# Performance work log

Hardware: AMD Instinct MI355X
Metric: run time of the kernel (lower is better)

The kernel has to match this reference:

```python
import jax, jax.numpy as jnp
import numpy as np


def setup_inputs() -> dict:
    key = jax.random.key(0)
    k1, k2 = jax.random.split(key)
    visual_features = jax.random.normal(k1, (16, 1024, 768), dtype=jnp.float32)
    text_tokens = jax.random.normal(k2, (16, 256, 768), dtype=jnp.float32)
    return {"visual_features": visual_features, "text_tokens": text_tokens, "k": 16}


def reference(visual_features, text_tokens, k):
    B, N, D = visual_features.shape
    T = min(k, N)

    # normalize (note: norm + 1e-6 in denominator, matching torch code)
    vis_norm = visual_features / (jnp.linalg.norm(visual_features, axis=-1, keepdims=True) + 1e-6)
    vis_norm = vis_norm.astype(jnp.float32)
    txt_norm = text_tokens / (jnp.linalg.norm(text_tokens, axis=-1, keepdims=True) + 1e-6)
    txt_norm = txt_norm.astype(jnp.float32)

    similarity = jnp.einsum('bnd,bmd->bnm', vis_norm, vis_norm)          # (B,N,N)
    relevance = jnp.einsum('bnd,btd->bnt', vis_norm, txt_norm).max(-1)    # (B,N)
    r_min = relevance.min(axis=1, keepdims=True)
    r_max = relevance.max(axis=1, keepdims=True)
    relevance = (relevance - r_min + 1e-6) / (r_max - r_min + 1e-6)

    kernel = relevance[:, :, None] * similarity * relevance[:, None, :]   # (B,N,N)

    di2s0 = jnp.diagonal(kernel, axis1=1, axis2=2)                        # (B,N)
    cis0 = jnp.zeros((T, B, N), dtype=kernel.dtype)
    barange = jnp.arange(B)

    def step(carry, i):
        di2s, cis = carry
        safe = jnp.maximum(di2s, 1e-12)
        j = jnp.argmax(safe, axis=-1)                                     # (B,)
        k_j = jnp.take_along_axis(kernel, j[:, None, None], axis=1)[:, 0, :]  # (B,N)
        dj = jnp.take_along_axis(di2s, j[:, None], axis=1)[:, 0]          # (B,)
        denom = jnp.sqrt(jnp.maximum(dj, 1e-12))[:, None] + 1e-8          # (B,1)
        # cis rows >= i are zero, so full-T contraction equals contraction over :i
        c_tb = jnp.take_along_axis(cis, j[None, :, None], axis=2)[:, :, 0]  # (T,B)
        cov = jnp.einsum('tb,tbn->bn', c_tb, cis)                         # (B,N)
        eis = (k_j - cov) / denom                                         # (B,N)
        cis = jax.lax.dynamic_update_index_in_dim(cis, eis, i, axis=0)
        di2s = di2s - eis ** 2
        di2s = di2s.at[barange, j].set(-jnp.inf)
        return (di2s, cis), j

    (_, _), sel = jax.lax.scan(step, (di2s0, cis0), jnp.arange(T))        # sel: (T,B)
    select_idx = jnp.sort(sel.T, axis=1)                                  # (B,T)
    selected = jnp.take_along_axis(visual_features, select_idx[:, :, None], axis=1)  # (B,T,D)
    if T < k:
        pad = jnp.zeros((B, k - T, D), dtype=selected.dtype)
        selected = jnp.concatenate([selected, pad], axis=1)
    return selected
```

## Files before the change

### kernel.cpp

```cpp
#include <hip/hip_runtime.h>
#include <math.h>

#define NB 16
#define NN 1024
#define ND 768
#define NT 256
#define NSEL 16
#define NC 64

typedef __attribute__((ext_vector_type(8))) short short8;
typedef __attribute__((ext_vector_type(4))) float f32x4;
typedef __attribute__((ext_vector_type(8))) unsigned short ushort8v;
typedef unsigned long long u64;

__device__ __align__(16) float g_invv[NB*NN];
__device__ __align__(16) float g_diagv[NB*NN];
__device__ __align__(16) float g_mrawp[NB*NN*2];
__device__ __align__(16) ushort8v g_tf[NB*2*24*2*8*64];

__device__ __forceinline__ unsigned short f2bf(float x) {
    unsigned u = __float_as_uint(x);
    return (unsigned short)((u + 0x7FFFu + ((u >> 16) & 1u)) >> 16);
}
__device__ __forceinline__ float bf2f(unsigned short h) {
    return __uint_as_float(((unsigned)h) << 16);
}
__device__ __forceinline__ size_t tfidx(int b, int th, int s, int h, int ct, int lane) {
    return ((((size_t)(b*2 + th)*24 + s)*2 + h)*8 + ct)*64 + lane;
}

__global__ __launch_bounds__(256) void ktxt(const float* __restrict__ txt) {
    int gw = (blockIdx.x * 256 + threadIdx.x) >> 6;
    int l  = threadIdx.x & 63;
    int b  = gw >> 8, r = gw & 255;
    int th = r >> 7, ct = (r >> 4) & 7, rlo = r & 15;
    const float* row = txt + (size_t)gw * ND;

    float4 x0 = *(const float4*)(row + 8*l);
    float4 y0 = *(const float4*)(row + 8*l + 4);
    float4 x1 = {0,0,0,0}, y1 = {0,0,0,0};
    bool two = (l < 32);
    if (two) {
        x1 = *(const float4*)(row + 512 + 8*l);
        y1 = *(const float4*)(row + 512 + 8*l + 4);
    }
    float s = x0.x*x0.x + x0.y*x0.y + x0.z*x0.z + x0.w*x0.w
            + y0.x*y0.x + y0.y*y0.y + y0.z*y0.z + y0.w*y0.w;
    if (two) s += x1.x*x1.x + x1.y*x1.y + x1.z*x1.z + x1.w*x1.w
                + y1.x*y1.x + y1.y*y1.y + y1.z*y1.z + y1.w*y1.w;
    #pragma unroll
    for (int off = 32; off; off >>= 1) s += __shfl_xor(s, off);
    float inv = 1.0f / (sqrtf(s) + 1e-6f);

    int kslot = l & 3;
    int lane  = kslot*16 + rlo;
    {
        int st = l >> 2;
        float a[8] = {x0.x, x0.y, x0.z, x0.w, y0.x, y0.y, y0.z, y0.w};
        ushort8v hh, ll;
        #pragma unroll
        for (int j = 0; j < 8; j++) {
            float v = a[j] * inv;
            hh[j] = f2bf(v);
            ll[j] = f2bf(v - bf2f(hh[j]));
        }
        g_tf[tfidx(b, th, st, 0, ct, lane)] = hh;
        g_tf[tfidx(b, th, st, 1, ct, lane)] = ll;
    }
    if (two) {
        int st = 16 + (l >> 2);
        float a[8] = {x1.x, x1.y, x1.z, x1.w, y1.x, y1.y, y1.z, y1.w};
        ushort8v hh, ll;
        #pragma unroll
        for (int j = 0; j < 8; j++) {
            float v = a[j] * inv;
            hh[j] = f2bf(v);
            ll[j] = f2bf(v - bf2f(hh[j]));
        }
        g_tf[tfidx(b, th, st, 0, ct, lane)] = hh;
        g_tf[tfidx(b, th, st, 1, ct, lane)] = ll;
    }
}

__global__ __launch_bounds__(256) void krel(const float* __restrict__ vis) {
    int bid = blockIdx.x;
    int lid = (bid & 7) * 64 + (bid >> 3);
    int b   = lid >> 5;
    int mt  = (lid >> 1) & 15;
    int th  = lid & 1;
    int t   = threadIdx.x;
    int w   = t >> 6, l = t & 63;

    __shared__ __align__(16) ushort8v Bfrag[3][2][8][64];

    f32x4 acc[8];
    #pragma unroll
    for (int ct = 0; ct < 8; ct++) acc[ct] = (f32x4){0.f, 0.f, 0.f, 0.f};

    int arow = mt*64 + w*16 + (l & 15);
    int akq  = (l >> 4) * 8;
    const float* Ap = vis + ((size_t)(b*NN + arow))*ND + akq;

    const ushort8v* Bbase = g_tf + tfidx(b, th, 0, 0, 0, 0);

    #define STAGE(S, P)                                                          \
        {                                                                        \
            _Pragma("unroll")                                                    \
            for (int q = 0; q < 4; q++) {                                        \
                int c  = w*4 + q;                                                \
                int h  = c >> 3, ct = c & 7;                                     \
                const ushort8v* gsrc = Bbase + (((size_t)(S)*2 + h)*8 + ct)*64 + l; \
                __builtin_amdgcn_global_load_lds(                                \
                    (const __attribute__((address_space(1))) void*)gsrc,         \
                    (__attribute__((address_space(3))) void*)&Bfrag[P][h][ct][0],\
                    16, 0, 0);                                                   \
            }                                                                    \
        }

    float4 rax = *(const float4*)(Ap);
    float4 ray = *(const float4*)(Ap + 4);
    STAGE(0, 0);
    STAGE(1, 1);
    __syncthreads();
    float ss = 0.f;

    for (int s = 0; s < 24; s++) {
        int p = s % 3;
        int k0 = s * 32;
        if (s < 22) STAGE(s + 2, (s + 2) % 3);
        asm volatile("" ::: "memory");
        float av[8] = {rax.x, rax.y, rax.z, rax.w, ray.x, ray.y, ray.z, ray.w};
        ushort8v hh, ll;
        #pragma unroll
        for (int j = 0; j < 8; j++) {
            hh[j] = f2bf(av[j]);
            ll[j] = f2bf(av[j] - bf2f(hh[j]));
            ss = fmaf(av[j], av[j], ss);
        }
        short8 ah = *(short8*)&hh;
        short8 al = *(short8*)&ll;
        if (s < 23) {
            rax = *(const float4*)(Ap + k0 + 32);
            ray = *(const float4*)(Ap + k0 + 36);
        }
        #pragma unroll
        for (int ct = 0; ct < 8; ct++) {
            short8 bh = *(const short8*)&Bfrag[p][0][ct][l];
            short8 bl = *(const short8*)&Bfrag[p][1][ct][l];
            acc[ct] = __builtin_amdgcn_mfma_f32_16x16x32_bf16(ah, bh, acc[ct], 0, 0, 0);
            acc[ct] = __builtin_amdgcn_mfma_f32_16x16x32_bf16(al, bh, acc[ct], 0, 0, 0);
            acc[ct] = __builtin_amdgcn_mfma_f32_16x16x32_bf16(ah, bl, acc[ct], 0, 0, 0);
            acc[ct] = __builtin_amdgcn_mfma_f32_16x16x32_bf16(al, bl, acc[ct], 0, 0, 0);
        }
        if (s < 23) {
            asm volatile("s_waitcnt lgkmcnt(0)" ::: "memory");
            __builtin_amdgcn_s_barrier();
            __builtin_amdgcn_sched_barrier(0);
        }
    }
    #undef STAGE

    #pragma unroll
    for (int r = 0; r < 4; r++) {
        float m = acc[0][r];
        #pragma unroll
        for (int ct = 1; ct < 8; ct++) m = fmaxf(m, acc[ct][r]);
        #pragma unroll
        for (int off = 1; off <= 8; off <<= 1) m = fmaxf(m, __shfl_xor(m, off));
        if ((l & 15) == 0)
            g_mrawp[(size_t)(b*NN + mt*64 + w*16 + (l >> 4)*4 + r)*2 + th] = m;
    }

    ss += __shfl_xor(ss, 16);
    ss += __shfl_xor(ss, 32);
    if (th == 0 && l < 16) {
        int row = mt*64 + w*16 + l;
        float nrm = sqrtf(ss);
        float inv = 1.0f / (nrm + 1e-6f);
        g_invv[b*NN + row] = inv;
        float dd = nrm * inv;
        g_diagv[b*NN + row] = dd * dd;
    }
}

__global__ __launch_bounds__(1024) void kfinal(const float* __restrict__ vis,
                                               float* __restrict__ out) {
    int b = blockIdx.x;
    int t = threadIdx.x;
    int w = t >> 6, l = t & 63;

    __shared__ u64   s_key[NN];
    __shared__ float s_reln[NN];
    __shared__ __align__(16) unsigned short Chi[NC][392], Clo[NC][392];
    __shared__ float s_S[NC*65];
    __shared__ int   s_sel[NSEL], s_srt[NSEL];
    __shared__ float s_mn[16], s_mx[16], s_b2[2];

    float m0 = g_mrawp[(size_t)(b*NN + t)*2 + 0];
    float m1 = g_mrawp[(size_t)(b*NN + t)*2 + 1];
    float iv = g_invv[b*NN + t], dd = g_diagv[b*NN + t];
    float rr = fmaxf(m0, m1) * iv;
    float lmin = rr, lmax = rr;
    #pragma unroll
    for (int off = 32; off; off >>= 1) {
        lmin = fminf(lmin, __shfl_xor(lmin, off));
        lmax = fmaxf(lmax, __shfl_xor(lmax, off));
    }
    if (l == 0) { s_mn[w] = lmin; s_mx[w] = lmax; }
    __syncthreads();
    if (t == 0) {
        float mn = s_mn[0], mx = s_mx[0];
        #pragma unroll
        for (int q = 1; q < 16; q++) { mn = fminf(mn, s_mn[q]); mx = fmaxf(mx, s_mx[q]); }
        s_b2[0] = mn; s_b2[1] = mx;
    }
    __syncthreads();
    float mn = s_b2[0], mx = s_b2[1];
    float den = mx - mn + 1e-6f;
    float rn = (rr - mn + 1e-6f) / den;
    float d0 = rn * rn * dd;
    s_reln[t] = rn;
    u64 kreg = ((u64)(~__float_as_uint(d0)) << 10) | (unsigned)t;

    #pragma unroll
    for (int k = 2; k <= 64; k <<= 1) {
        #pragma unroll
        for (int j = k >> 1; j > 0; j >>= 1) {
            u64 part = __shfl_xor(kreg, j);
            bool takeMin = ((l & k) == 0) == ((l & j) == 0);
            kreg = takeMin ? (kreg < part ? kreg : part) : (kreg < part ? part : kreg);
        }
    }
    #pragma unroll
    for (int rnd = 0; rnd < 4; rnd++) {
        int dstp = 8 >> rnd;
        s_key[w*64 + l] = kreg;
        __syncthreads();
        u64 other = s_key[(w ^ dstp)*64 + (63 - l)];
        u64 m = (kreg < other) ? kreg : other;
        #pragma unroll
        for (int j = 32; j > 0; j >>= 1) {
            u64 part = __shfl_xor(m, j);
            bool takeMin = ((l & j) == 0);
            m = takeMin ? (m < part ? m : part) : (m < part ? part : m);
        }
        kreg = m;
        __syncthreads();
    }

    int   gid = (int)(kreg & 1023u);
    float d0v = __uint_as_float(~(unsigned)(kreg >> 10));

    f32x4 acc = (f32x4){0.f, 0.f, 0.f, 0.f};
    int ar0 = (w >> 2) * 16, bc0 = (w & 3) * 16;
    int cr  = (w << 2) + (l >> 4);
    int sgid = __shfl(gid, cr);
    float sc = g_invv[b*NN + sgid];
    const float* srcrow = vis + (size_t)(b*NN + sgid)*ND + (l & 15)*24;

    for (int c = 0; c < 2; c++) {
        __syncthreads();
        int kb = (l & 15) * 24;
        #pragma unroll
        for (int q = 0; q < 3; q++) {
            float4 x = *(const float4*)(srcrow + c*384 + q*8);
            float4 y = *(const float4*)(srcrow + c*384 + q*8 + 4);
            float av[8] = {x.x, x.y, x.z, x.w, y.x, y.y, y.z, y.w};
            ushort8v hh, ll;
            #pragma unroll
            for (int j = 0; j < 8; j++) {
                float vv = av[j] * sc;
                hh[j] = f2bf(vv);
                ll[j] = f2bf(vv - bf2f(hh[j]));
            }
            *(ushort8v*)&Chi[cr][kb + q*8] = hh;
            *(ushort8v*)&Clo[cr][kb + q*8] = ll;
        }
        __syncthreads();
        #pragma unroll
        for (int ks = 0; ks < 12; ks++) {
            int ko = ks*32 + (l >> 4)*8;
            short8 ah = *(const short8*)&Chi[ar0 + (l & 15)][ko];
            short8 al = *(const short8*)&Clo[ar0 + (l & 15)][ko];
            short8 bh = *(const short8*)&Chi[bc0 + (l & 15)][ko];
            short8 bl = *(const short8*)&Clo[bc0 + (l & 15)][ko];
            acc = __builtin_amdgcn_mfma_f32_16x16x32_bf16(ah, bh, acc, 0, 0, 0);
            acc = __builtin_amdgcn_mfma_f32_16x16x32_bf16(al, bh, acc, 0, 0, 0);
            acc = __builtin_amdgcn_mfma_f32_16x16x32_bf16(ah, bl, acc, 0, 0, 0);
            acc = __builtin_amdgcn_mfma_f32_16x16x32_bf16(al, bl, acc, 0, 0, 0);
        }
    }
    #pragma unroll
    for (int r = 0; r < 4; r++)
        s_S[(ar0 + (l >> 4)*4 + r)*65 + bc0 + (l & 15)] = acc[r];
    __syncthreads();

    if (w == 0) {
        float di  = d0v;
        int   gd  = gid;
        float rel = s_reln[gid];
        float ownc[NSEL];
        #pragma unroll
        for (int i = 0; i < NSEL; i++) {
            float vq = fmaxf(di, 1e-12f);
            int   gq = gd;
            int   cq = l;
            #pragma unroll
            for (int off = 32; off; off >>= 1) {
                float vo = __shfl_xor(vq, off);
                int   go = __shfl_xor(gq, off);
                int   co = __shfl_xor(cq, off);
                if (vo > vq || (vo == vq && go < gq)) { vq = vo; gq = go; cq = co; }
            }
            float dj   = __shfl(di, cq);
            float relj = __shfl(rel, cq);
            float denom = sqrtf(fmaxf(dj, 1e-12f)) + 1e-8f;
            if (l == 0) s_sel[i] = gq;

            float cov = 0.f;
            #pragma unroll
            for (int q = 0; q < i; q++)
                cov = fmaf(ownc[q], __shfl(ownc[q], cq), cov);

            float sim = s_S[l*65 + cq];
            float kj  = rel * relj * sim;
            float eis = (kj - cov) / denom;
            ownc[i] = eis;
            di = di - eis * eis;
            if (l == cq) di = -__builtin_inff();
        }
    }
    __syncthreads();

    if (t == 0) {
        int vv[16];
        #pragma unroll
        for (int q = 0; q < 16; q++) vv[q] = s_sel[q];
        for (int a = 1; a < 16; a++) {
            int key = vv[a]; int p2 = a - 1;
            while (p2 >= 0 && vv[p2] > key) { vv[p2+1] = vv[p2]; p2--; }
            vv[p2+1] = key;
        }
        #pragma unroll
        for (int q = 0; q < 16; q++) s_srt[q] = vv[q];
    }
    __syncthreads();
    {
        int idx = s_srt[w];
        const float* src = vis + (size_t)(b*NN + idx)*ND + l*12;
        float*       dst = out + (size_t)(b*NSEL + w)*ND + l*12;
        float4 x = *(const float4*)(src);
        float4 y = *(const float4*)(src + 4);
        float4 z = *(const float4*)(src + 8);
        *(float4*)(dst)     = x;
        *(float4*)(dst + 4) = y;
        *(float4*)(dst + 8) = z;
    }
}

extern "C" void kernel_launch(void* const* d_in, const int* in_sizes, int n_in,
                              void* d_out, int out_size, void* d_ws, size_t ws_size,
                              hipStream_t stream) {
    (void)in_sizes; (void)n_in; (void)d_ws; (void)ws_size; (void)out_size;
    const float* vis = (const float*)d_in[0];
    const float* txt = (const float*)d_in[1];
    float* out = (float*)d_out;

    ktxt  <<<dim3((NB*NT)/4), dim3(256),  0, stream>>>(txt);
    krel  <<<dim3(512),       dim3(256),  0, stream>>>(vis);
    kfinal<<<dim3(NB),        dim3(1024), 0, stream>>>(vis, out);
}
```

Baseline: 72.21 us.

## Double krel row tile per wave and load B fragments directly from global

The relevance GEMM kernel now has each wave compute 32 visual rows instead of 16. This halves the grid to 256 blocks and reuses each B fragment across two A tiles. The LDS triple-buffered staging via global_load_lds is replaced by direct per-lane global loads of the text fragments into registers, which removes the LDS traffic and waitcnt. The cost is more registers per thread, a one-block-per-CU occupancy hint, and loss of the prefetch pipeline for B.

```diff
diff --git a/kernel.cpp b/kernel.cpp
--- a/kernel.cpp
+++ b/kernel.cpp
@@ -82,105 +82,110 @@
     }
 }
 
-__global__ __launch_bounds__(256) void krel(const float* __restrict__ vis) {
+__global__ __launch_bounds__(256, 1) void krel(const float* __restrict__ vis) {
     int bid = blockIdx.x;
-    int lid = (bid & 7) * 64 + (bid >> 3);
-    int b   = lid >> 5;
-    int mt  = (lid >> 1) & 15;
-    int th  = lid & 1;
+    int lid = (bid & 7) * 32 + (bid >> 3);
+    int b   = lid >> 4;
+    int r   = lid & 15;
+    int mt  = r >> 1;
+    int th  = r & 1;
     int t   = threadIdx.x;
     int w   = t >> 6, l = t & 63;
 
-    __shared__ __align__(16) ushort8v Bfrag[3][2][8][64];
-
-    f32x4 acc[8];
-    #pragma unroll
-    for (int ct = 0; ct < 8; ct++) acc[ct] = (f32x4){0.f, 0.f, 0.f, 0.f};
-
-    int arow = mt*64 + w*16 + (l & 15);
-    int akq  = (l >> 4) * 8;
-    const float* Ap = vis + ((size_t)(b*NN + arow))*ND + akq;
-
-    const ushort8v* Bbase = g_tf + tfidx(b, th, 0, 0, 0, 0);
-
-    #define STAGE(S, P)                                                          \
-        {                                                                        \
-            _Pragma("unroll")                                                    \
-            for (int q = 0; q < 4; q++) {                                        \
-                int c  = w*4 + q;                                                \
-                int h  = c >> 3, ct = c & 7;                                     \
-                const ushort8v* gsrc = Bbase + (((size_t)(S)*2 + h)*8 + ct)*64 + l; \
-                __builtin_amdgcn_global_load_lds(                                \
-                    (const __attribute__((address_space(1))) void*)gsrc,         \
-                    (__attribute__((address_space(3))) void*)&Bfrag[P][h][ct][0],\
-                    16, 0, 0);                                                   \
-            }                                                                    \
-        }
-
-    float4 rax = *(const float4*)(Ap);
-    float4 ray = *(const float4*)(Ap + 4);
-    STAGE(0, 0);
-    STAGE(1, 1);
-    __syncthreads();
-    float ss = 0.f;
+    f32x4 acc0[8], acc1[8];
+    #pragma unroll
+    for (int ct = 0; ct < 8; ct++) {
+        acc0[ct] = (f32x4){0.f, 0.f, 0.f, 0.f};
+        acc1[ct] = (f32x4){0.f, 0.f, 0.f, 0.f};
+    }
+
+    int base = mt*128 + w*32;
+    const float* Ap0 = vis + ((size_t)(b*NN + base + (l & 15)))*ND + (l >> 4)*8;
+    const float* Ap1 = Ap0 + (size_t)16*ND;
+
+    const ushort8v* Bb = g_tf + (size_t)(b*2 + th)*(24*2*8*64) + l;
+
+    float4 a0x = *(const float4*)(Ap0);
+    float4 a0y = *(const float4*)(Ap0 + 4);
+    float4 a1x = *(const float4*)(Ap1);
+    float4 a1y = *(const float4*)(Ap1 + 4);
+    float ss0 = 0.f, ss1 = 0.f;
+
+    #define CONV8(AX, AY, AH, AL, SS)                                          \
+        {                                                                      \
+            float av_[8] = {AX.x, AX.y, AX.z, AX.w, AY.x, AY.y, AY.z, AY.w};   \
+            ushort8v hh_, ll_;                                                 \
+            _Pragma("unroll")                                                  \
+            for (int j = 0; j < 8; j++) {                                      \
+                hh_[j] = f2bf(av_[j]);                                         \
+                ll_[j] = f2bf(av_[j] - bf2f(hh_[j]));                          \
+                SS = fmaf(av_[j], av_[j], SS);                                 \
+            }                                                                  \
+            AH = *(short8*)&hh_;                                               \
+            AL = *(short8*)&ll_;                                               \
+        }
+
+    #define MM(ACC, AA, BB)                                                    \
+        _Pragma("unroll")                                                      \
+        for (int ct = 0; ct < 8; ct++)                                         \
+            ACC[ct] = __builtin_amdgcn_mfma_f32_16x16x32_bf16(                 \
+                AA, *(short8*)&BB[ct], ACC[ct], 0, 0, 0);
 
     for (int s = 0; s < 24; s++) {
-        int p = s % 3;
-        int k0 = s * 32;
-        if (s < 22) STAGE(s + 2, (s + 2) % 3);
-        asm volatile("" ::: "memory");
-        float av[8] = {rax.x, rax.y, rax.z, rax.w, ray.x, ray.y, ray.z, ray.w};
-        ushort8v hh, ll;
-        #pragma unroll
-        for (int j = 0; j < 8; j++) {
-            hh[j] = f2bf(av[j]);
-            ll[j] = f2bf(av[j] - bf2f(hh[j]));
-            ss = fmaf(av[j], av[j], ss);
-        }
-        short8 ah = *(short8*)&hh;
-        short8 al = *(short8*)&ll;
+        const ushort8v* Bs = Bb + (size_t)s*(2*8*64);
+        ushort8v bh[8], blv[8];
+        #pragma unroll
+        for (int ct = 0; ct < 8; ct++) {
+            bh[ct]  = Bs[ct*64];
+            blv[ct] = Bs[(8 + ct)*64];
+        }
+        float4 n0x, n0y, n1x, n1y;
         if (s < 23) {
-            rax = *(const float4*)(Ap + k0 + 32);
-            ray = *(const float4*)(Ap + k0 + 36);
-        }
-        #pragma unroll
-        for (int ct = 0; ct < 8; ct++) {
-            short8 bh = *(const short8*)&Bfrag[p][0][ct][l];
-            short8 bl = *(const short8*)&Bfrag[p][1][ct][l];
-            acc[ct] = __builtin_amdgcn_mfma_f32_16x16x32_bf16(ah, bh, acc[ct], 0, 0, 0);
-            acc[ct] = __builtin_amdgcn_mfma_f32_16x16x32_bf16(al, bh, acc[ct], 0, 0, 0);
-            acc[ct] = __builtin_amdgcn_mfma_f32_16x16x32_bf16(ah, bl, acc[ct], 0, 0, 0);
-            acc[ct] = __builtin_amdgcn_mfma_f32_16x16x32_bf16(al, bl, acc[ct], 0, 0, 0);
-        }
-        if (s < 23) {
-            asm volatile("s_waitcnt lgkmcnt(0)" ::: "memory");
-            __builtin_amdgcn_s_barrier();
-            __builtin_amdgcn_sched_barrier(0);
-        }
-    }
-    #undef STAGE
-
-    #pragma unroll
-    for (int r = 0; r < 4; r++) {
-        float m = acc[0][r];
-        #pragma unroll
-        for (int ct = 1; ct < 8; ct++) m = fmaxf(m, acc[ct][r]);
-        #pragma unroll
-        for (int off = 1; off <= 8; off <<= 1) m = fmaxf(m, __shfl_xor(m, off));
-        if ((l & 15) == 0)
-            g_mrawp[(size_t)(b*NN + mt*64 + w*16 + (l >> 4)*4 + r)*2 + th] = m;
-    }
-
-    ss += __shfl_xor(ss, 16);
-    ss += __shfl_xor(ss, 32);
-    if (th == 0 && l < 16) {
-        int row = mt*64 + w*16 + l;
-        float nrm = sqrtf(ss);
-        float inv = 1.0f / (nrm + 1e-6f);
-        g_invv[b*NN + row] = inv;
-        float dd = nrm * inv;
-        g_diagv[b*NN + row] = dd * dd;
-    }
+            int k1 = (s + 1) * 32;
+            n0x = *(const float4*)(Ap0 + k1);
+            n0y = *(const float4*)(Ap0 + k1 + 4);
+            n1x = *(const float4*)(Ap1 + k1);
+            n1y = *(const float4*)(Ap1 + k1 + 4);
+        }
+        short8 ah0, al0, ah1, al1;
+        CONV8(a0x, a0y, ah0, al0, ss0);
+        CONV8(a1x, a1y, ah1, al1, ss1);
+        MM(acc0, ah0, bh)  MM(acc0, al0, bh)  MM(acc0, ah0, blv)  MM(acc0, al0, blv)
+        MM(acc1, ah1, bh)  MM(acc1, al1, bh)  MM(acc1, ah1, blv)  MM(acc1, al1, blv)
+        if (s < 23) { a0x = n0x; a0y = n0y; a1x = n1x; a1y = n1y; }
+        __builtin_amdgcn_s_barrier();
+    }
+    #undef MM
+    #undef CONV8
+
+    #define EPI(ACC, MOFF, SS)                                                 \
+        {                                                                      \
+            _Pragma("unroll")                                                  \
+            for (int rr = 0; rr < 4; rr++) {                                   \
+                float mx_ = ACC[0][rr];                                        \
+                _Pragma("unroll")                                              \
+                for (int ct = 1; ct < 8; ct++) mx_ = fmaxf(mx_, ACC[ct][rr]);  \
+                _Pragma("unroll")                                              \
+                for (int off = 1; off <= 8; off <<= 1)                         \
+                    mx_ = fmaxf(mx_, __shfl_xor(mx_, off));                    \
+                if ((l & 15) == 0)                                             \
+                    g_mrawp[(size_t)(b*NN + base + (MOFF) + (l >> 4)*4 + rr)*2 + th] = mx_; \
+            }                                                                  \
+            float sst_ = SS;                                                   \
+            sst_ += __shfl_xor(sst_, 16);                                      \
+            sst_ += __shfl_xor(sst_, 32);                                      \
+            if (th == 0 && l < 16) {                                           \
+                int row_ = base + (MOFF) + l;                                  \
+                float nrm_ = sqrtf(sst_);                                      \
+                float inv_ = 1.0f / (nrm_ + 1e-6f);                            \
+                g_invv[b*NN + row_] = inv_;                                    \
+                float dd_ = nrm_ * inv_;                                       \
+                g_diagv[b*NN + row_] = dd_ * dd_;                              \
+            }                                                                  \
+        }
+    EPI(acc0, 0,  ss0)
+    EPI(acc1, 16, ss1)
+    #undef EPI
 }
 
 __global__ __launch_bounds__(1024) void kfinal(const float* __restrict__ vis,
@@ -367,6 +372,6 @@
     float* out = (float*)d_out;
 
     ktxt  <<<dim3((NB*NT)/4), dim3(256),  0, stream>>>(txt);
-    krel  <<<dim3(512),       dim3(256),  0, stream>>>(vis);
+    krel  <<<dim3(256),       dim3(256),  0, stream>>>(vis);
     kfinal<<<dim3(NB),        dim3(1024), 0, stream>>>(vis, out);
 }
```

New measurement: 82.00 us. +13.5%, slower.

## Split relevance GEMM text columns four ways to double krel block count

Applied to the files above, without the earlier changes.

The krel relevance kernel now gives each block 64 text tokens instead of 128, so the grid doubles from 512 to 1024 blocks. The per-row max partials widen from 2 to 4 slots, and kfinal reduces all four. Launch bounds request 4 blocks per SM, and the LDS staging and accumulators shrink by half. The aim is more parallelism and occupancy on a GPU with many CUs, at the cost of reading the visual A rows and converting them to bf16 twice as often.

```diff
diff --git a/kernel.cpp b/kernel.cpp
--- a/kernel.cpp
+++ b/kernel.cpp
@@ -15,7 +15,7 @@
 
 __device__ __align__(16) float g_invv[NB*NN];
 __device__ __align__(16) float g_diagv[NB*NN];
-__device__ __align__(16) float g_mrawp[NB*NN*2];
+__device__ __align__(16) float g_mrawp[NB*NN*4];
 __device__ __align__(16) ushort8v g_tf[NB*2*24*2*8*64];
 
 __device__ __forceinline__ unsigned short f2bf(float x) {
@@ -82,37 +82,39 @@
     }
 }
 
-__global__ __launch_bounds__(256) void krel(const float* __restrict__ vis) {
+__global__ __launch_bounds__(256, 4) void krel(const float* __restrict__ vis) {
     int bid = blockIdx.x;
-    int lid = (bid & 7) * 64 + (bid >> 3);
-    int b   = lid >> 5;
-    int mt  = (lid >> 1) & 15;
-    int th  = lid & 1;
+    int lid = (bid & 7) * 128 + (bid >> 3);
+    int b   = lid >> 6;
+    int rem = lid & 63;
+    int mt  = rem >> 2;
+    int q   = rem & 3;
+    int th  = q >> 1;
+    int cb  = (q & 1) * 4;
     int t   = threadIdx.x;
     int w   = t >> 6, l = t & 63;
 
-    __shared__ __align__(16) ushort8v Bfrag[3][2][8][64];
-
-    f32x4 acc[8];
-    #pragma unroll
-    for (int ct = 0; ct < 8; ct++) acc[ct] = (f32x4){0.f, 0.f, 0.f, 0.f};
+    __shared__ __align__(16) ushort8v Bfrag[3][2][4][64];
+
+    f32x4 acc[4];
+    #pragma unroll
+    for (int ct = 0; ct < 4; ct++) acc[ct] = (f32x4){0.f, 0.f, 0.f, 0.f};
 
     int arow = mt*64 + w*16 + (l & 15);
-    int akq  = (l >> 4) * 8;
-    const float* Ap = vis + ((size_t)(b*NN + arow))*ND + akq;
-
-    const ushort8v* Bbase = g_tf + tfidx(b, th, 0, 0, 0, 0);
+    const float* Ap = vis + ((size_t)(b*NN + arow))*ND + (l >> 4)*8;
+
+    const ushort8v* Bbase = g_tf + (size_t)(b*2 + th)*(24*2*8*64);
 
     #define STAGE(S, P)                                                          \
         {                                                                        \
             _Pragma("unroll")                                                    \
-            for (int q = 0; q < 4; q++) {                                        \
-                int c  = w*4 + q;                                                \
-                int h  = c >> 3, ct = c & 7;                                     \
-                const ushort8v* gsrc = Bbase + (((size_t)(S)*2 + h)*8 + ct)*64 + l; \
+            for (int qq = 0; qq < 2; qq++) {                                     \
+                int c   = w*2 + qq;                                              \
+                int h   = c >> 2, ctl = c & 3;                                   \
+                const ushort8v* gsrc = Bbase + (((size_t)(S)*2 + h)*8 + cb + ctl)*64 + l; \
                 __builtin_amdgcn_global_load_lds(                                \
                     (const __attribute__((address_space(1))) void*)gsrc,         \
-                    (__attribute__((address_space(3))) void*)&Bfrag[P][h][ct][0],\
+                    (__attribute__((address_space(3))) void*)&Bfrag[P][h][ctl][0],\
                     16, 0, 0);                                                   \
             }                                                                    \
         }
@@ -144,7 +146,7 @@
             ray = *(const float4*)(Ap + k0 + 36);
         }
         #pragma unroll
-        for (int ct = 0; ct < 8; ct++) {
+        for (int ct = 0; ct < 4; ct++) {
             short8 bh = *(const short8*)&Bfrag[p][0][ct][l];
             short8 bl = *(const short8*)&Bfrag[p][1][ct][l];
             acc[ct] = __builtin_amdgcn_mfma_f32_16x16x32_bf16(ah, bh, acc[ct], 0, 0, 0);
@@ -164,16 +166,16 @@
     for (int r = 0; r < 4; r++) {
         float m = acc[0][r];
         #pragma unroll
-        for (int ct = 1; ct < 8; ct++) m = fmaxf(m, acc[ct][r]);
+        for (int ct = 1; ct < 4; ct++) m = fmaxf(m, acc[ct][r]);
         #pragma unroll
         for (int off = 1; off <= 8; off <<= 1) m = fmaxf(m, __shfl_xor(m, off));
         if ((l & 15) == 0)
-            g_mrawp[(size_t)(b*NN + mt*64 + w*16 + (l >> 4)*4 + r)*2 + th] = m;
+            g_mrawp[(size_t)(b*NN + mt*64 + w*16 + (l >> 4)*4 + r)*4 + q] = m;
     }
 
     ss += __shfl_xor(ss, 16);
     ss += __shfl_xor(ss, 32);
-    if (th == 0 && l < 16) {
+    if (q == 0 && l < 16) {
         int row = mt*64 + w*16 + l;
         float nrm = sqrtf(ss);
         float inv = 1.0f / (nrm + 1e-6f);
@@ -196,10 +198,12 @@
     __shared__ int   s_sel[NSEL], s_srt[NSEL];
     __shared__ float s_mn[16], s_mx[16], s_b2[2];
 
-    float m0 = g_mrawp[(size_t)(b*NN + t)*2 + 0];
-    float m1 = g_mrawp[(size_t)(b*NN + t)*2 + 1];
+    float m0 = g_mrawp[(size_t)(b*NN + t)*4 + 0];
+    float m1 = g_mrawp[(size_t)(b*NN + t)*4 + 1];
+    float m2 = g_mrawp[(size_t)(b*NN + t)*4 + 2];
+    float m3 = g_mrawp[(size_t)(b*NN + t)*4 + 3];
     float iv = g_invv[b*NN + t], dd = g_diagv[b*NN + t];
-    float rr = fmaxf(m0, m1) * iv;
+    float rr = fmaxf(fmaxf(m0, m1), fmaxf(m2, m3)) * iv;
     float lmin = rr, lmax = rr;
     #pragma unroll
     for (int off = 32; off; off >>= 1) {
@@ -211,7 +215,7 @@
     if (t == 0) {
         float mn = s_mn[0], mx = s_mx[0];
         #pragma unroll
-        for (int q = 1; q < 16; q++) { mn = fminf(mn, s_mn[q]); mx = fmaxf(mx, s_mx[q]); }
+        for (int qq = 1; qq < 16; qq++) { mn = fminf(mn, s_mn[qq]); mx = fmaxf(mx, s_mx[qq]); }
         s_b2[0] = mn; s_b2[1] = mx;
     }
     __syncthreads();
@@ -262,9 +266,9 @@
         __syncthreads();
         int kb = (l & 15) * 24;
         #pragma unroll
-        for (int q = 0; q < 3; q++) {
-            float4 x = *(const float4*)(srcrow + c*384 + q*8);
-            float4 y = *(const float4*)(srcrow + c*384 + q*8 + 4);
+        for (int qq = 0; qq < 3; qq++) {
+            float4 x = *(const float4*)(srcrow + c*384 + qq*8);
+            float4 y = *(const float4*)(srcrow + c*384 + qq*8 + 4);
             float av[8] = {x.x, x.y, x.z, x.w, y.x, y.y, y.z, y.w};
             ushort8v hh, ll;
             #pragma unroll
@@ -273,8 +277,8 @@
                 hh[j] = f2bf(vv);
                 ll[j] = f2bf(vv - bf2f(hh[j]));
             }
-            *(ushort8v*)&Chi[cr][kb + q*8] = hh;
-            *(ushort8v*)&Clo[cr][kb + q*8] = ll;
+            *(ushort8v*)&Chi[cr][kb + qq*8] = hh;
+            *(ushort8v*)&Clo[cr][kb + qq*8] = ll;
         }
         __syncthreads();
         #pragma unroll
@@ -319,8 +323,8 @@
 
             float cov = 0.f;
             #pragma unroll
-            for (int q = 0; q < i; q++)
-                cov = fmaf(ownc[q], __shfl(ownc[q], cq), cov);
+            for (int qq = 0; qq < i; qq++)
+                cov = fmaf(ownc[qq], __shfl(ownc[qq], cq), cov);
 
             float sim = s_S[l*65 + cq];
             float kj  = rel * relj * sim;
@@ -335,14 +339,14 @@
     if (t == 0) {
         int vv[16];
         #pragma unroll
-        for (int q = 0; q < 16; q++) vv[q] = s_sel[q];
+        for (int qq = 0; qq < 16; qq++) vv[qq] = s_sel[qq];
         for (int a = 1; a < 16; a++) {
             int key = vv[a]; int p2 = a - 1;
             while (p2 >= 0 && vv[p2] > key) { vv[p2+1] = vv[p2]; p2--; }
             vv[p2+1] = key;
         }
         #pragma unroll
-        for (int q = 0; q < 16; q++) s_srt[q] = vv[q];
+        for (int qq = 0; qq < 16; qq++) s_srt[qq] = vv[qq];
     }
     __syncthreads();
     {
@@ -367,6 +371,6 @@
     float* out = (float*)d_out;
 
     ktxt  <<<dim3((NB*NT)/4), dim3(256),  0, stream>>>(txt);
-    krel  <<<dim3(512),       dim3(256),  0, stream>>>(vis);
+    krel  <<<dim3(1024),      dim3(256),  0, stream>>>(vis);
     kfinal<<<dim3(NB),        dim3(1024), 0, stream>>>(vis, out);
 }
```

New measurement: 75.95 us. +5.2%, slower.
